# Kernel optimization log

Hardware: AMD Instinct MI355X
Metric: run time of the kernel (lower is better)

## Reference

```python
import jax, jax.numpy as jnp
import numpy as np

NX, NY, C, B, P = 432, 496, 64, 4, 40000


def setup_inputs() -> dict:
    key = jax.random.key(0)
    k1, _ = jax.random.split(key)
    pillar_features = jax.random.normal(k1, (P, C), dtype=jnp.float32)
    # Build voxel_coords with unique (x, y) cells per batch element so the
    # scatter-write has no duplicate indices (matches deterministic torch assignment).
    rng = np.random.default_rng(0)
    per = P // B  # pillars per sample
    coords = np.empty((P, 3), dtype=np.int64)
    for b in range(B):
        flat = rng.choice(NX * NY, size=per, replace=False)
        coords[b * per:(b + 1) * per, 0] = flat % NX          # x index
        coords[b * per:(b + 1) * per, 1] = flat // NX         # y index
        coords[b * per:(b + 1) * per, 2] = b                  # batch index (last col)
    return {
        "pillar_features": pillar_features,
        "voxel_coords": jnp.asarray(coords),
        "batch_size": B,
        "nx": NX,
        "ny": NY,
    }


def reference(pillar_features, voxel_coords, batch_size, nx, ny):
    # Fused scatter: compute a global flat index (batch, y, x) for every pillar
    # and scatter all pillars in a single pass (no per-batch masking loop).
    x = voxel_coords[:, 0]
    y = voxel_coords[:, 1]
    b = voxel_coords[:, -1]
    flat = b * (ny * nx) + y * nx + x                       # [P]
    c = pillar_features.shape[1]
    grid = jnp.zeros((batch_size * ny * nx, c), dtype=pillar_features.dtype)
    grid = grid.at[flat].set(pillar_features)               # scatter pillars
    # [B*ny*nx, C] -> [B, C, ny, nx]
    return grid.reshape(batch_size, ny, nx, c).transpose(0, 3, 1, 2)
```

## Files before the change

kernel.cpp:

```cpp
#include <hip/hip_runtime.h>


#define C_CH 64

typedef float nat_float4 __attribute__((ext_vector_type(4)));

__global__ void build_map_kernel(const int* __restrict__ coords, int n_pillars,
                                 const int* __restrict__ nx_p,
                                 const int* __restrict__ ny_p,
                                 int* __restrict__ map) {
    int p = blockIdx.x * blockDim.x + threadIdx.x;
    if (p >= n_pillars) return;
    const int nx = nx_p[0];
    const int ny = ny_p[0];
    const int x = coords[3 * p + 0];
    const int y = coords[3 * p + 1];
    const int b = coords[3 * p + 2];
    const long long m = (long long)b * (long long)(nx * ny) + (long long)y * nx + x;
    map[m] = p;
}

__global__ void __launch_bounds__(256) gather_linear_kernel(
        const float* __restrict__ feat,
        const int* __restrict__ map,
        const int* __restrict__ nx_p,
        const int* __restrict__ ny_p,
        float* __restrict__ out, int n_out4) {
    const int t = blockIdx.x * blockDim.x + threadIdx.x;
    if (t >= n_out4) return;
    const int plane4 = (nx_p[0] * ny_p[0]) >> 2;

    const int bc  = t / plane4;
    const int yx4 = t - bc * plane4;
    const int b   = bc >> 6;
    const int c   = bc & 63;

    const int4 pv = ((const int4*)map)[b * plane4 + yx4];

    nat_float4 v = {0.f, 0.f, 0.f, 0.f};
    if (pv.x >= 0) v.x = feat[pv.x * C_CH + c];
    if (pv.y >= 0) v.y = feat[pv.y * C_CH + c];
    if (pv.z >= 0) v.z = feat[pv.z * C_CH + c];
    if (pv.w >= 0) v.w = feat[pv.w * C_CH + c];

    __builtin_nontemporal_store(v, ((nat_float4*)out) + t);
}

__global__ void direct_scatter_kernel(const float* __restrict__ feat,
                                      const int* __restrict__ coords,
                                      int n_pillars, int C,
                                      const int* __restrict__ nx_p,
                                      const int* __restrict__ ny_p,
                                      float* __restrict__ out) {
    const long long t = (long long)blockIdx.x * blockDim.x + threadIdx.x;
    if (t >= (long long)n_pillars * C) return;
    const int p = (int)(t / C);
    const int c = (int)(t - (long long)p * C);
    const int nx = nx_p[0];
    const int ny = ny_p[0];
    const int x = coords[3 * p + 0];
    const int y = coords[3 * p + 1];
    const int b = coords[3 * p + 2];
    const int plane = nx * ny;
    const size_t o = ((size_t)b * C + c) * (size_t)plane + (size_t)y * nx + x;
    out[o] = feat[(size_t)p * C + c];
}

extern "C" void kernel_launch(void* const* d_in, const int* in_sizes, int n_in,
                              void* d_out, int out_size, void* d_ws, size_t ws_size,
                              hipStream_t stream) {
    const float* feat   = (const float*)d_in[0];
    const int*   coords = (const int*)d_in[1];
    const int* nx_p = (const int*)d_in[3];
    const int* ny_p = (const int*)d_in[4];
    float* out = (float*)d_out;

    const int n_pillars = in_sizes[1] / 3;
    const int C = in_sizes[0] / n_pillars;
    const int n_map = out_size / C;
    const size_t map_bytes = (size_t)n_map * sizeof(int);

    if (C == C_CH && (n_map & 3) == 0 && (out_size & 3) == 0 &&
        ws_size >= map_bytes) {
        int* map = (int*)d_ws;
        (void)hipMemsetAsync(map, 0xFF, map_bytes, stream);
        build_map_kernel<<<(n_pillars + 255) / 256, 256, 0, stream>>>(
            coords, n_pillars, nx_p, ny_p, map);
        const int n_out4 = out_size >> 2;
        gather_linear_kernel<<<(n_out4 + 255) / 256, 256, 0, stream>>>(
            feat, map, nx_p, ny_p, out, n_out4);
    } else {
        (void)hipMemsetAsync(out, 0, (size_t)out_size * sizeof(float), stream);
        const long long total = (long long)n_pillars * C;
        direct_scatter_kernel<<<(unsigned)((total + 255) / 256), 256, 0, stream>>>(
            feat, coords, n_pillars, C, nx_p, ny_p, out);
    }
}
```

Measured before the change: 242.4 us.

## Gather 16 channels per thread with vectorized feature row loads

```diff
diff --git a/kernel.cpp b/kernel.cpp
--- a/kernel.cpp
+++ b/kernel.cpp
@@ -20,30 +20,55 @@
     map[m] = p;
 }
 
-__global__ void __launch_bounds__(256) gather_linear_kernel(
+__global__ void __launch_bounds__(256) gather16_kernel(
         const float* __restrict__ feat,
         const int* __restrict__ map,
         const int* __restrict__ nx_p,
         const int* __restrict__ ny_p,
-        float* __restrict__ out, int n_out4) {
+        float* __restrict__ out, int n_thread) {
     const int t = blockIdx.x * blockDim.x + threadIdx.x;
-    if (t >= n_out4) return;
+    if (t >= n_thread) return;
     const int plane4 = (nx_p[0] * ny_p[0]) >> 2;
+    const int bcg = t / plane4;
+    const int i   = t - bcg * plane4;
+    const int b   = bcg >> 2;
+    const int cgrp = bcg & 3;
 
-    const int bc  = t / plane4;
-    const int yx4 = t - bc * plane4;
-    const int b   = bc >> 6;
-    const int c   = bc & 63;
+    const int4 pv = ((const int4*)map)[b * plane4 + i];
 
-    const int4 pv = ((const int4*)map)[b * plane4 + yx4];
+    const nat_float4 zero = {0.f, 0.f, 0.f, 0.f};
+    nat_float4 fx[4], fy[4], fz[4], fw[4];
+#pragma unroll
+    for (int k = 0; k < 4; ++k) { fx[k] = zero; fy[k] = zero; fz[k] = zero; fw[k] = zero; }
 
-    nat_float4 v = {0.f, 0.f, 0.f, 0.f};
-    if (pv.x >= 0) v.x = feat[pv.x * C_CH + c];
-    if (pv.y >= 0) v.y = feat[pv.y * C_CH + c];
-    if (pv.z >= 0) v.z = feat[pv.z * C_CH + c];
-    if (pv.w >= 0) v.w = feat[pv.w * C_CH + c];
+    const nat_float4* __restrict__ f4 = (const nat_float4*)feat;
+    if (pv.x >= 0) {
+        const nat_float4* r = f4 + pv.x * (C_CH / 4) + cgrp * 4;
+        fx[0] = r[0]; fx[1] = r[1]; fx[2] = r[2]; fx[3] = r[3];
+    }
+    if (pv.y >= 0) {
+        const nat_float4* r = f4 + pv.y * (C_CH / 4) + cgrp * 4;
+        fy[0] = r[0]; fy[1] = r[1]; fy[2] = r[2]; fy[3] = r[3];
+    }
+    if (pv.z >= 0) {
+        const nat_float4* r = f4 + pv.z * (C_CH / 4) + cgrp * 4;
+        fz[0] = r[0]; fz[1] = r[1]; fz[2] = r[2]; fz[3] = r[3];
+    }
+    if (pv.w >= 0) {
+        const nat_float4* r = f4 + pv.w * (C_CH / 4) + cgrp * 4;
+        fw[0] = r[0]; fw[1] = r[1]; fw[2] = r[2]; fw[3] = r[3];
+    }
 
-    __builtin_nontemporal_store(v, ((nat_float4*)out) + t);
+    nat_float4* __restrict__ o = (nat_float4*)out + ((b * C_CH + cgrp * 16) * plane4 + i);
+#pragma unroll
+    for (int kk = 0; kk < 4; ++kk) {
+#pragma unroll
+        for (int j = 0; j < 4; ++j) {
+            nat_float4 v;
+            v.x = fx[kk][j]; v.y = fy[kk][j]; v.z = fz[kk][j]; v.w = fw[kk][j];
+            o[(kk * 4 + j) * plane4] = v;
+        }
+    }
 }
 
 __global__ void direct_scatter_kernel(const float* __restrict__ feat,
@@ -86,9 +111,9 @@
         (void)hipMemsetAsync(map, 0xFF, map_bytes, stream);
         build_map_kernel<<<(n_pillars + 255) / 256, 256, 0, stream>>>(
             coords, n_pillars, nx_p, ny_p, map);
-        const int n_out4 = out_size >> 2;
-        gather_linear_kernel<<<(n_out4 + 255) / 256, 256, 0, stream>>>(
-            feat, map, nx_p, ny_p, out, n_out4);
+        const int n_thread = n_map;
+        gather16_kernel<<<(n_thread + 255) / 256, 256, 0, stream>>>(
+            feat, map, nx_p, ny_p, out, n_thread);
     } else {
         (void)hipMemsetAsync(out, 0, (size_t)out_size * sizeof(float), stream);
         const long long total = (long long)n_pillars * C;
```

Measured after the change: 233.4 us. -3.7%, faster.
